# Optimization experiments

Measured on AMD Instinct MI355X. Metric: run time of the kernel, lower is better.

The kernel has to match this reference:

```python
import jax, jax.numpy as jnp
import numpy as np
import math

EPS = 1e-5

def setnorm(x, w, b):
    # normalize over (samples, features) per batch element, then per-feature scale/shift
    m = jnp.mean(x, axis=(1, 2), keepdims=True)
    s = jnp.sqrt(jnp.mean(jnp.square(x - m), axis=(1, 2), keepdims=True) + EPS)
    return (x - m) / s * w + b

def setup_inputs() -> dict:
    key = jax.random.key(0)
    ks = jax.random.split(key, 8)
    B, Nx, Ny, dX, dY = 4, 2048, 2048, 256, 256
    sX, sY = 1.0 / math.sqrt(dX), 1.0 / math.sqrt(dY)
    return {
        'X': jax.random.normal(ks[0], (B, Nx, dX), jnp.float32),
        'Y': jax.random.normal(ks[1], (B, Ny, dY), jnp.float32),
        'Wq': jax.random.normal(ks[2], (dY, dX), jnp.float32) * sX,
        'bq': jnp.zeros((dY,), jnp.float32),
        'Wk': jax.random.normal(ks[3], (dY, dY), jnp.float32) * sY,
        'bk': jnp.zeros((dY,), jnp.float32),
        'Wv': jax.random.normal(ks[4], (dY, dY), jnp.float32) * sY,
        'bv': jnp.zeros((dY,), jnp.float32),
        'Wo': jax.random.normal(ks[5], (dX, dY), jnp.float32) * sY,
        'bo': jnp.zeros((dX,), jnp.float32),
        'Wres': jax.random.normal(ks[6], (dX, dX), jnp.float32) * sX,
        'bres': jnp.zeros((dX,), jnp.float32),
        'nq_w': jnp.ones((dX,), jnp.float32), 'nq_b': jnp.zeros((dX,), jnp.float32),
        'nk_w': jnp.ones((dY,), jnp.float32), 'nk_b': jnp.zeros((dY,), jnp.float32),
        'n0_w': jnp.ones((dX,), jnp.float32), 'n0_b': jnp.zeros((dX,), jnp.float32),
    }

def reference(X, Y, Wq, bq, Wk, bk, Wv, bv, Wo, bo, Wres, bres,
              nq_w, nq_b, nk_w, nk_b, n0_w, n0_b):
    num_heads = 8
    dim_Y = Wq.shape[0]
    d = dim_Y // num_heads
    B, Nx, _ = X.shape
    Ny = Y.shape[1]

    Q = setnorm(X, nq_w, nq_b) @ Wq.T + bq          # [B, Nx, dY]
    K = setnorm(Y, nk_w, nk_b) @ Wk.T + bk          # [B, Ny, dY]
    V = Y @ Wv.T + bv                               # [B, Ny, dY]

    # split into heads along feature dim (matches torch split/cat over dim 0)
    Qh = Q.reshape(B, Nx, num_heads, d)
    Kh = K.reshape(B, Ny, num_heads, d)
    Vh = V.reshape(B, Ny, num_heads, d)

    # NOTE: original scales by sqrt(dim_Y), not sqrt(head_dim)
    scores = jnp.einsum('bqhd,bkhd->bhqk', Qh, Kh) / math.sqrt(dim_Y)
    A = jax.nn.softmax(scores, axis=-1)             # [B, H, Nx, Ny]
    Oh = jnp.einsum('bhqk,bkhd->bqhd', A, Vh)       # [B, Nx, H, d]
    O = Oh.reshape(B, Nx, dim_Y) @ Wo.T + bo        # [B, Nx, dX]

    H = X + O
    H = H + jax.nn.relu(setnorm(H, n0_w, n0_b)) @ Wres.T + bres
    return H
```

## Files before the change

### kernel.cpp

```cpp
#include <hip/hip_runtime.h>


typedef _Float16 f16;
typedef _Float16 f16x4 __attribute__((ext_vector_type(4)));
typedef _Float16 f16x8 __attribute__((ext_vector_type(8)));
typedef float f32x4 __attribute__((ext_vector_type(4)));
typedef float f32x16 __attribute__((ext_vector_type(16)));
typedef unsigned int u32;
typedef unsigned int u32x2 __attribute__((ext_vector_type(2)));
typedef unsigned int u32x4 __attribute__((ext_vector_type(4)));

#define DEV static __device__ __forceinline__

DEV void load_lds16(const void* g, void* s) {
  __builtin_amdgcn_global_load_lds(
      (const __attribute__((address_space(1))) void*)g,
      (__attribute__((address_space(3))) void*)s, 16, 0, 0);
}

DEV float fexp2(float x) {
  float r;
  asm("v_exp_f32 %0, %1" : "=v"(r) : "v"(x));
  return r;
}

DEV u32 pkh(float a, float b) {
  auto h = __builtin_amdgcn_cvt_pkrtz(a, b);
  return __builtin_bit_cast(u32, h);
}

__global__ __launch_bounds__(256) void stats_partial(const float* __restrict__ p0,
                                                     const float* __restrict__ p1,
                                                     float2* __restrict__ partial) {
  const int s = blockIdx.y;
  const float* p = (s >= 4 ? p1 + (size_t)(s - 4) * 524288 : p0 + (size_t)s * 524288)
                   + (size_t)blockIdx.x * 8192;
  float sum = 0.f, ss = 0.f;
#pragma unroll
  for (int j = 0; j < 8; ++j) {
    f32x4 v = *reinterpret_cast<const f32x4*>(p + (size_t)(j * 256 + threadIdx.x) * 4);
#pragma unroll
    for (int e = 0; e < 4; ++e) { sum += v[e]; ss += v[e] * v[e]; }
  }
#pragma unroll
  for (int m = 1; m < 64; m <<= 1) { sum += __shfl_xor(sum, m); ss += __shfl_xor(ss, m); }
  __shared__ float2 red[4];
  if ((threadIdx.x & 63) == 0) red[threadIdx.x >> 6] = make_float2(sum, ss);
  __syncthreads();
  if (threadIdx.x == 0) {
    float a = 0.f, b = 0.f;
    for (int i = 0; i < 4; ++i) { a += red[i].x; b += red[i].y; }
    partial[s * 64 + blockIdx.x] = make_float2(a, b);
  }
}

DEV float2 finalize_stats(const float2* __restrict__ partial, int s) {
  const int lane = threadIdx.x & 63;
  float2 v = partial[s * 64 + lane];
  float sum = v.x, ss = v.y;
#pragma unroll
  for (int m = 1; m < 64; m <<= 1) { sum += __shfl_xor(sum, m); ss += __shfl_xor(ss, m); }
  const float invN = 1.f / 524288.f;
  const float mean = sum * invN;
  const float var = fmaxf(ss * invN - mean * mean, 0.f);
  return make_float2(mean, rsqrtf(var + 1e-5f));
}

__global__ __launch_bounds__(256) void prep_xy(const float* __restrict__ X,
                                               const float* __restrict__ Y,
                                               f16* __restrict__ Xn, f16* __restrict__ Yn,
                                               f16* __restrict__ Yc,
                                               const float2* __restrict__ partial,
                                               const float* __restrict__ nqw, const float* __restrict__ nqb,
                                               const float* __restrict__ nkw, const float* __restrict__ nkb) {
  const int bid = blockIdx.x;
  const bool isX = bid < 1024;
  const size_t idx = ((size_t)(isX ? bid : bid - 1024) * 256 + threadIdx.x) * 8;
  const int slice = (int)(idx >> 19);
  const float2 st = finalize_stats(partial, (isX ? 0 : 4) + slice);
  const int f = (int)(idx & 255);
  const float* in = isX ? X : Y;
  f32x4 v0 = *reinterpret_cast<const f32x4*>(in + idx);
  f32x4 v1 = *reinterpret_cast<const f32x4*>(in + idx + 4);
  const float* wv = isX ? nqw : nkw;
  const float* bv = isX ? nqb : nkb;
  f32x4 w0 = *reinterpret_cast<const f32x4*>(wv + f);
  f32x4 w1 = *reinterpret_cast<const f32x4*>(wv + f + 4);
  f32x4 b0 = *reinterpret_cast<const f32x4*>(bv + f);
  f32x4 b1 = *reinterpret_cast<const f32x4*>(bv + f + 4);
  f16x8 on;
#pragma unroll
  for (int j = 0; j < 4; ++j) {
    on[j]     = (f16)((v0[j] - st.x) * st.y * w0[j] + b0[j]);
    on[j + 4] = (f16)((v1[j] - st.x) * st.y * w1[j] + b1[j]);
  }
  if (isX) {
    *reinterpret_cast<f16x8*>(Xn + idx) = on;
  } else {
    *reinterpret_cast<f16x8*>(Yn + idx) = on;
    f16x8 oc;
#pragma unroll
    for (int j = 0; j < 4; ++j) { oc[j] = (f16)v0[j]; oc[j + 4] = (f16)v1[j]; }
    *reinterpret_cast<f16x8*>(Yc + idx) = oc;
  }
}

__global__ __launch_bounds__(256) void prep_h(const float* __restrict__ H, f16* __restrict__ out,
                                              const float2* __restrict__ partial,
                                              const float* __restrict__ w, const float* __restrict__ b) {
  const size_t idx = ((size_t)blockIdx.x * 256 + threadIdx.x) * 8;
  const float2 st = finalize_stats(partial, (int)(idx >> 19));
  const int f = (int)(idx & 255);
  f32x4 v0 = *reinterpret_cast<const f32x4*>(H + idx);
  f32x4 v1 = *reinterpret_cast<const f32x4*>(H + idx + 4);
  f32x4 w0 = *reinterpret_cast<const f32x4*>(w + f);
  f32x4 w1 = *reinterpret_cast<const f32x4*>(w + f + 4);
  f32x4 b0 = *reinterpret_cast<const f32x4*>(b + f);
  f32x4 b1 = *reinterpret_cast<const f32x4*>(b + f + 4);
  f16x8 o;
#pragma unroll
  for (int j = 0; j < 4; ++j) {
    o[j]     = (f16)fmaxf((v0[j] - st.x) * st.y * w0[j] + b0[j], 0.f);
    o[j + 4] = (f16)fmaxf((v1[j] - st.x) * st.y * w1[j] + b1[j], 0.f);
  }
  *reinterpret_cast<f16x8*>(out + idx) = o;
}

__global__ __launch_bounds__(256) void cast_w(const float* __restrict__ w0, const float* __restrict__ w1,
                                              const float* __restrict__ w2, const float* __restrict__ w3,
                                              const float* __restrict__ w4, f16* __restrict__ out) {
  const int i8 = blockIdx.x * 256 + threadIdx.x;
  const int mat = i8 >> 13;
  const size_t off = (size_t)(i8 & 8191) * 8;
  const float* src = mat == 0 ? w0 : mat == 1 ? w1 : mat == 2 ? w2 : mat == 3 ? w3 : w4;
  f32x4 v0 = *reinterpret_cast<const f32x4*>(src + off);
  f32x4 v1 = *reinterpret_cast<const f32x4*>(src + off + 4);
  f16x8 o;
#pragma unroll
  for (int j = 0; j < 4; ++j) { o[j] = (f16)v0[j]; o[j + 4] = (f16)v1[j]; }
  *reinterpret_cast<f16x8*>(out + (size_t)mat * 65536 + off) = o;
}

enum { GM_F16 = 0, GM_VT = 1, GM_F32R = 2 };

template <bool QKV>
__global__ __launch_bounds__(256) void gemm_nt(const f16* __restrict__ A0, const f16* __restrict__ A1,
                                               const f16* __restrict__ A2, const f16* __restrict__ Wc,
                                               const float* __restrict__ b0, const float* __restrict__ b1,
                                               const float* __restrict__ b2,
                                               const float* __restrict__ resid,
                                               void* o0p, void* o1p, void* o2p,
                                               float scale0, int mode0) {
  __shared__ __align__(16) f16 lds[2][8192];
  const int t = threadIdx.x;
  const int w = t >> 6, lane = t & 63;
  const int g = lane >> 4, lq = lane & 15;
  const int m0 = blockIdx.x * 64, n0 = blockIdx.y * 64;
  const int wr = (w >> 1) * 32, wc = (w & 1) * 32;
  const int z = QKV ? blockIdx.z : 0;

  const f16* A = QKV ? (z == 0 ? A0 : z == 1 ? A1 : A2) : A0;
  const f16* W = QKV ? (Wc + z * 65536) : Wc;
  const float* bias = QKV ? (z == 0 ? b0 : z == 1 ? b1 : b2) : b0;
  void* outp = QKV ? (z == 0 ? o0p : z == 1 ? o1p : o2p) : o0p;
  const float scale = (QKV && z != 0) ? 1.f : scale0;
  const int mode = QKV ? (z == 2 ? GM_VT : GM_F16) : mode0;

  const int r_ = t >> 2, c0 = t & 3, sw = (t >> 3) & 3;
  const int kgA = (c0 ^ sw) << 3;
  const f16* gA = A + (size_t)(m0 + r_) * 256 + kgA;
  const f16* gB = W + (size_t)(n0 + r_) * 256 + kgA;
  f16* dA0 = &lds[0][0] + t * 8;
  f16* dA1 = &lds[1][0] + t * 8;

  f32x4 acc[2][2] = {};

  auto stage = [&](int kt, int buf) {
    f16* base = buf ? dA1 : dA0;
    const int ko = kt * 64;
    load_lds16(gA + ko, base);
    load_lds16(gA + ko + 32, base + 2048);
    load_lds16(gB + ko, base + 4096);
    load_lds16(gB + ko + 32, base + 6144);
  };

  const int swr = ((lq >> 1) & 3);
  auto compute = [&](int buf) {
    const f16* L = &lds[buf][0];
#pragma unroll
    for (int kk = 0; kk < 2; ++kk) {
      f16x8 af[2], bf[2];
#pragma unroll
      for (int i = 0; i < 2; ++i)
        af[i] = *reinterpret_cast<const f16x8*>(L + kk * 2048 + (wr + i * 16 + lq) * 32 + ((g ^ swr) << 3));
#pragma unroll
      for (int j = 0; j < 2; ++j)
        bf[j] = *reinterpret_cast<const f16x8*>(L + 4096 + kk * 2048 + (wc + j * 16 + lq) * 32 + ((g ^ swr) << 3));
#pragma unroll
      for (int i = 0; i < 2; ++i)
#pragma unroll
        for (int j = 0; j < 2; ++j)
          acc[i][j] = __builtin_amdgcn_mfma_f32_16x16x32_f16(af[i], bf[j], acc[i][j], 0, 0, 0);
    }
  };

  stage(0, 0);
  __syncthreads();
  stage(1, 1); compute(0); __syncthreads();
  stage(2, 0); compute(1); __syncthreads();
  stage(3, 1); compute(0); __syncthreads();
  compute(1);

#pragma unroll
  for (int i = 0; i < 2; ++i)
#pragma unroll
    for (int j = 0; j < 2; ++j) {
      const int row0 = m0 + wr + i * 16 + g * 4;
      const int col = n0 + wc + j * 16 + lq;
      const float bv = bias[col];
#pragma unroll
      for (int r = 0; r < 4; ++r) {
        const int rr = row0 + r;
        float v = (acc[i][j][r] + bv) * scale;
        if (mode == GM_F16) {
          ((f16*)outp)[(size_t)rr * 256 + col] = (f16)v;
        } else if (mode == GM_VT) {
          ((f16*)outp)[((size_t)(rr >> 11) * 256 + col) * 2048 + (rr & 2047)] = (f16)v;
        } else {
          const size_t o = (size_t)rr * 256 + col;
          ((float*)outp)[o] = v + resid[o];
        }
      }
    }
}

__global__ __launch_bounds__(256) void attn_kernel(const f16* __restrict__ Q,
                                                   const f16* __restrict__ K,
                                                   const f16* __restrict__ Vt,
                                                   f16* __restrict__ O) {
  __shared__ __align__(16) f16 kbuf[2][2048];
  __shared__ __align__(16) f16 vbuf[2][2048];
  const int t = threadIdx.x;
  const int w = t >> 6, lane = t & 63;
  const int l31 = lane & 31, hi = lane >> 5;
  const int wg = blockIdx.x;
  const int linear = (wg & 7) * 64 + (wg >> 3);
  const int qt = linear & 15;
  const int hb = linear >> 4;
  const int h = hb & 7, b = hb >> 3;
  const int q0 = qt * 128 + w * 32;

  const f16* Kb = K + (size_t)b * 2048 * 256 + h * 32;
  const f16* Vb = Vt + ((size_t)b * 256 + h * 32) * 2048;

  const f16* qp = Q + (size_t)(b * 2048 + q0 + l31) * 256 + h * 32 + hi * 8;
  const f16x8 qf0 = *reinterpret_cast<const f16x8*>(qp);
  const f16x8 qf1 = *reinterpret_cast<const f16x8*>(qp + 16);

  const f16* gK = Kb + (size_t)(t >> 2) * 256 + (((t & 3) ^ ((t >> 2) & 3)) << 3);
  const f16* gV = Vb + (size_t)(t >> 3) * 2048 + (((t & 7) ^ ((t >> 3) & 7)) << 3);
  f16* dKa = &kbuf[0][0] + t * 8;
  f16* dKb = &kbuf[1][0] + t * 8;
  f16* dVa = &vbuf[0][0] + t * 8;
  f16* dVb = &vbuf[1][0] + t * 8;
  const int KSTEP = 64 * 256;

  const int kR = l31 * 32, kx = l31 & 3;
  const int vR = l31 * 64, vx = l31 & 7;

  f32x16 acc = {};
  float l_ = 0.f;
  const f32x16 zz = {};

  auto compute = [&](int buf) {
    const f16* kb = buf ? &kbuf[1][0] : &kbuf[0][0];
    const f16* vb = buf ? &vbuf[1][0] : &vbuf[0][0];
    f16x8 vf[4];
#pragma unroll
    for (int kc = 0; kc < 4; ++kc)
      vf[kc] = *reinterpret_cast<const f16x8*>(vb + vR + ((((kc << 1) | hi) ^ vx) << 3));

#pragma unroll
    for (int kh = 0; kh < 2; ++kh) {
      f16x8 kf0 = *reinterpret_cast<const f16x8*>(kb + kh * 1024 + kR + ((hi ^ kx) << 3));
      f16x8 kf1 = *reinterpret_cast<const f16x8*>(kb + kh * 1024 + kR + (((2 | hi) ^ kx) << 3));
      __builtin_amdgcn_s_setprio(1);
      f32x16 s = __builtin_amdgcn_mfma_f32_32x32x16_f16(kf0, qf0, zz, 0, 0, 0);
      s = __builtin_amdgcn_mfma_f32_32x32x16_f16(kf1, qf1, s, 0, 0, 0);
      __builtin_amdgcn_s_setprio(0);

      float e[16];
#pragma unroll
      for (int i = 0; i < 16; ++i) e[i] = fexp2(s[i]);
      float sa = ((e[0] + e[1]) + (e[2] + e[3])) + ((e[4] + e[5]) + (e[6] + e[7]));
      float sb = ((e[8] + e[9]) + (e[10] + e[11])) + ((e[12] + e[13]) + (e[14] + e[15]));
      l_ += sa + sb;

      u32 pk0 = pkh(e[0], e[1]),   pk1 = pkh(e[2], e[3]);
      u32 pk2 = pkh(e[4], e[5]),   pk3 = pkh(e[6], e[7]);
      u32 pk4 = pkh(e[8], e[9]),   pk5 = pkh(e[10], e[11]);
      u32 pk6 = pkh(e[12], e[13]), pk7 = pkh(e[14], e[15]);

      u32 a0 = pk0, b0 = pk2;
      asm("v_permlane32_swap_b32 %0, %1" : "+v"(a0), "+v"(b0));
      u32 a1 = pk1, b1 = pk3;
      asm("v_permlane32_swap_b32 %0, %1" : "+v"(a1), "+v"(b1));
      u32 c0 = pk4, d0 = pk6;
      asm("v_permlane32_swap_b32 %0, %1" : "+v"(c0), "+v"(d0));
      u32 c1 = pk5, d1 = pk7;
      asm("v_permlane32_swap_b32 %0, %1" : "+v"(c1), "+v"(d1));
      u32x4 paAw = {a0, a1, b0, b1};
      u32x4 paBw = {c0, c1, d0, d1};
      f16x8 paA = __builtin_bit_cast(f16x8, paAw);
      f16x8 paB = __builtin_bit_cast(f16x8, paBw);

      __builtin_amdgcn_s_setprio(1);
      acc = __builtin_amdgcn_mfma_f32_32x32x16_f16(paA, vf[kh * 2 + 0], acc, 0, 0, 0);
      acc = __builtin_amdgcn_mfma_f32_32x32x16_f16(paB, vf[kh * 2 + 1], acc, 0, 0, 0);
      __builtin_amdgcn_s_setprio(0);
    }
  };

  load_lds16(gK, dKa);
  load_lds16(gV, dVa);
  gK += KSTEP; gV += 64;
  __syncthreads();

  for (int kt = 0; kt < 32; kt += 2) {
    load_lds16(gK, dKb);
    load_lds16(gV, dVb);
    gK += KSTEP; gV += 64;
    compute(0);
    __syncthreads();
    if (kt < 30) {
      load_lds16(gK, dKa);
      load_lds16(gV, dVa);
      gK += KSTEP; gV += 64;
    }
    compute(1);
    __syncthreads();
  }

  float lf = l_ + __shfl_xor(l_, 32);
  const float inv = 1.f / lf;
#pragma unroll
  for (int i = 0; i < 16; ++i) {
    const int ql = (i & 3) + ((i >> 2) << 3) + (hi << 2);
    const float invq = __shfl(inv, ql);
    const size_t row = (size_t)b * 2048 + q0 + ql;
    O[row * 256 + h * 32 + l31] = (f16)(acc[i] * invq);
  }
}

extern "C" void kernel_launch(void* const* d_in, const int* in_sizes, int n_in,
                              void* d_out, int out_size, void* d_ws, size_t ws_size,
                              hipStream_t stream) {
  (void)in_sizes; (void)n_in; (void)out_size; (void)ws_size;
  const float* X    = (const float*)d_in[0];
  const float* Y    = (const float*)d_in[1];
  const float* Wq   = (const float*)d_in[2];
  const float* bq   = (const float*)d_in[3];
  const float* Wk   = (const float*)d_in[4];
  const float* bk   = (const float*)d_in[5];
  const float* Wv   = (const float*)d_in[6];
  const float* bv   = (const float*)d_in[7];
  const float* Wo   = (const float*)d_in[8];
  const float* bo   = (const float*)d_in[9];
  const float* Wres = (const float*)d_in[10];
  const float* bres = (const float*)d_in[11];
  const float* nq_w = (const float*)d_in[12];
  const float* nq_b = (const float*)d_in[13];
  const float* nk_w = (const float*)d_in[14];
  const float* nk_b = (const float*)d_in[15];
  const float* n0_w = (const float*)d_in[16];
  const float* n0_b = (const float*)d_in[17];
  float* out = (float*)d_out;

  char* ws = (char*)d_ws;
  const size_t MB = 1u << 20;
  f16* bufXn = (f16*)(ws + 0 * MB);
  f16* bufYn = (f16*)(ws + 4 * MB);
  f16* bufYc = (f16*)(ws + 8 * MB);
  f16* bufQ  = (f16*)(ws + 12 * MB);
  f16* bufK  = (f16*)(ws + 16 * MB);
  f16* bufVt = (f16*)(ws + 20 * MB);
  f16* bufW  = (f16*)(ws + 24 * MB);
  float2* partial = (float2*)(ws + 24 * MB + 700 * 1024);

  stats_partial<<<dim3(64, 8), 256, 0, stream>>>(X, Y, partial);

  cast_w<<<160, 256, 0, stream>>>(Wq, Wk, Wv, Wo, Wres, bufW);
  prep_xy<<<2048, 256, 0, stream>>>(X, Y, bufXn, bufYn, bufYc, partial,
                                    nq_w, nq_b, nk_w, nk_b);

  const float qscale = 1.4426950408889634f / 16.f;
  gemm_nt<true><<<dim3(128, 4, 3), 256, 0, stream>>>(
      bufXn, bufYn, bufYc, bufW, bq, bk, bv, nullptr,
      bufQ, bufK, bufVt, qscale, GM_F16);

  attn_kernel<<<512, 256, 0, stream>>>(bufQ, bufK, bufVt, bufXn);

  gemm_nt<false><<<dim3(128, 4), 256, 0, stream>>>(
      bufXn, nullptr, nullptr, bufW + 3 * 65536, bo, nullptr, nullptr, X,
      out, nullptr, nullptr, 1.f, GM_F32R);

  stats_partial<<<dim3(64, 4), 256, 0, stream>>>(out, out, partial);
  prep_h<<<1024, 256, 0, stream>>>(out, bufYc, partial, n0_w, n0_b);

  gemm_nt<false><<<dim3(128, 4), 256, 0, stream>>>(
      bufYc, nullptr, nullptr, bufW + 4 * 65536, bres, nullptr, nullptr, out,
      out, nullptr, nullptr, 1.f, GM_F32R);
}
```

Baseline: 96.14 us.

## Split attention key range across wave pairs and double the grid

Each attention workgroup now covers 64 queries instead of 128. Its four waves form two query sub-tiles times two key halves, and each workgroup stages both key/value halves into LDS together. The two key-half partial accumulators and row sums are merged through LDS at the end. This works because the softmax has no running max (the exponentials are plain exp2), so the partial sums can simply be added. The grid goes from 512 to 1024 workgroups to give more parallelism on the many CUs. The cost is that each K/V tile is loaded twice as often per query, LDS use is doubled, and the kernel gains an extra reduction step.

Result: faster. 91.15 us (-5.2%).

```diff
diff --git a/kernel.cpp b/kernel.cpp
--- a/kernel.cpp
+++ b/kernel.cpp
@@ -234,21 +234,22 @@
     }
 }
 
-__global__ __launch_bounds__(256) void attn_kernel(const f16* __restrict__ Q,
-                                                   const f16* __restrict__ K,
-                                                   const f16* __restrict__ Vt,
-                                                   f16* __restrict__ O) {
-  __shared__ __align__(16) f16 kbuf[2][2048];
-  __shared__ __align__(16) f16 vbuf[2][2048];
+__global__ __launch_bounds__(256, 4) void attn_kernel(const f16* __restrict__ Q,
+                                                      const f16* __restrict__ K,
+                                                      const f16* __restrict__ Vt,
+                                                      f16* __restrict__ O) {
+  __shared__ __align__(16) f16 kbuf[2][2][2048];
+  __shared__ __align__(16) f16 vbuf[2][2][2048];
   const int t = threadIdx.x;
   const int w = t >> 6, lane = t & 63;
   const int l31 = lane & 31, hi = lane >> 5;
+  const int qsub = w & 1, khalf = w >> 1;
   const int wg = blockIdx.x;
-  const int linear = (wg & 7) * 64 + (wg >> 3);
-  const int qt = linear & 15;
-  const int hb = linear >> 4;
+  const int linear = (wg & 7) * 128 + (wg >> 3);
+  const int qt = linear & 31;
+  const int hb = linear >> 5;
   const int h = hb & 7, b = hb >> 3;
-  const int q0 = qt * 128 + w * 32;
+  const int q0 = qt * 64 + qsub * 32;
 
   const f16* Kb = K + (size_t)b * 2048 * 256 + h * 32;
   const f16* Vb = Vt + ((size_t)b * 256 + h * 32) * 2048;
@@ -259,11 +260,9 @@
 
   const f16* gK = Kb + (size_t)(t >> 2) * 256 + (((t & 3) ^ ((t >> 2) & 3)) << 3);
   const f16* gV = Vb + (size_t)(t >> 3) * 2048 + (((t & 7) ^ ((t >> 3) & 7)) << 3);
-  f16* dKa = &kbuf[0][0] + t * 8;
-  f16* dKb = &kbuf[1][0] + t * 8;
-  f16* dVa = &vbuf[0][0] + t * 8;
-  f16* dVb = &vbuf[1][0] + t * 8;
   const int KSTEP = 64 * 256;
+  const int KH = 16 * KSTEP;
+  const int VH = 16 * 64;
 
   const int kR = l31 * 32, kx = l31 & 3;
   const int vR = l31 * 64, vx = l31 & 7;
@@ -272,9 +271,19 @@
   float l_ = 0.f;
   const f32x16 zz = {};
 
+  auto stage = [&](int buf) {
+    f16* kd = buf ? &kbuf[1][0][0] : &kbuf[0][0][0];
+    f16* vd = buf ? &vbuf[1][0][0] : &vbuf[0][0][0];
+    load_lds16(gK,      kd + t * 8);
+    load_lds16(gK + KH, kd + 2048 + t * 8);
+    load_lds16(gV,      vd + t * 8);
+    load_lds16(gV + VH, vd + 2048 + t * 8);
+    gK += KSTEP; gV += 64;
+  };
+
   auto compute = [&](int buf) {
-    const f16* kb = buf ? &kbuf[1][0] : &kbuf[0][0];
-    const f16* vb = buf ? &vbuf[1][0] : &vbuf[0][0];
+    const f16* kb = (buf ? &kbuf[1][0][0] : &kbuf[0][0][0]) + khalf * 2048;
+    const f16* vb = (buf ? &vbuf[1][0][0] : &vbuf[0][0][0]) + khalf * 2048;
     f16x8 vf[4];
 #pragma unroll
     for (int kc = 0; kc < 4; ++kc)
@@ -321,34 +330,39 @@
     }
   };
 
-  load_lds16(gK, dKa);
-  load_lds16(gV, dVa);
-  gK += KSTEP; gV += 64;
+  stage(0);
   __syncthreads();
 
-  for (int kt = 0; kt < 32; kt += 2) {
-    load_lds16(gK, dKb);
-    load_lds16(gV, dVb);
-    gK += KSTEP; gV += 64;
+  for (int st = 0; st < 16; st += 2) {
+    stage(1);
     compute(0);
     __syncthreads();
-    if (kt < 30) {
-      load_lds16(gK, dKa);
-      load_lds16(gV, dVa);
-      gK += KSTEP; gV += 64;
-    }
+    if (st < 14) stage(0);
     compute(1);
     __syncthreads();
   }
 
-  float lf = l_ + __shfl_xor(l_, 32);
-  const float inv = 1.f / lf;
-#pragma unroll
-  for (int i = 0; i < 16; ++i) {
-    const int ql = (i & 3) + ((i >> 2) << 3) + (hi << 2);
-    const float invq = __shfl(inv, ql);
-    const size_t row = (size_t)b * 2048 + q0 + ql;
-    O[row * 256 + h * 32 + l31] = (f16)(acc[i] * invq);
+  float* cb = reinterpret_cast<float*>(&kbuf[0][0][0]);
+  const int slot = (qsub * 64 + lane) * 17;
+  if (khalf == 1) {
+#pragma unroll
+    for (int i = 0; i < 16; ++i) cb[slot + i] = acc[i];
+    cb[slot + 16] = l_;
+  }
+  __syncthreads();
+  if (khalf == 0) {
+#pragma unroll
+    for (int i = 0; i < 16; ++i) acc[i] += cb[slot + i];
+    l_ += cb[slot + 16];
+    float lf = l_ + __shfl_xor(l_, 32);
+    const float inv = 1.f / lf;
+#pragma unroll
+    for (int i = 0; i < 16; ++i) {
+      const int ql = (i & 3) + ((i >> 2) << 3) + (hi << 2);
+      const float invq = __shfl(inv, ql);
+      const size_t row = (size_t)b * 2048 + q0 + ql;
+      O[row * 256 + h * 32 + l31] = (f16)(acc[i] * invq);
+    }
   }
 }
 
@@ -398,7 +412,7 @@
       bufXn, bufYn, bufYc, bufW, bq, bk, bv, nullptr,
       bufQ, bufK, bufVt, qscale, GM_F16);
 
-  attn_kernel<<<512, 256, 0, stream>>>(bufQ, bufK, bufVt, bufXn);
+  attn_kernel<<<1024, 256, 0, stream>>>(bufQ, bufK, bufVt, bufXn);
 
   gemm_nt<false><<<dim3(128, 4), 256, 0, stream>>>(
       bufXn, nullptr, nullptr, bufW + 3 * 65536, bo, nullptr, nullptr, X,
```
